# Performance work log

Measured on AMD Instinct MI355X. Metric: run time of the kernel, lower is better.

## Reference

```python
import jax, jax.numpy as jnp
import numpy as np

D_MODEL, N_HEADS, D_STATE, N_GROUPS, CHUNK = 2048, 32, 64, 1, 256
BATCH, SEQLEN = 2, 4096


def setup_inputs() -> dict:
    key = jax.random.key(0)
    ks = jax.random.split(key, 8)
    s = 0.02
    d, h, n, g = D_MODEL, N_HEADS, D_STATE, N_GROUPS
    return {
        "x": jax.random.normal(ks[0], (BATCH, SEQLEN, d), jnp.float32),
        "A_log": jnp.log(jnp.arange(1, h + 1, dtype=jnp.float32)),
        "D": jnp.ones((h,), jnp.float32),
        "B_w": jax.random.normal(ks[1], (g * n, d), jnp.float32) * s,
        "B_b": jnp.zeros((g * n,), jnp.float32),
        "C_w": jax.random.normal(ks[2], (g * n, d), jnp.float32) * s,
        "C_b": jnp.zeros((g * n,), jnp.float32),
        "dt_w": jax.random.normal(ks[3], (h, d), jnp.float32) * s,
        "dt_b": jnp.zeros((h,), jnp.float32),
        "out_w": jax.random.normal(ks[4], (d, d), jnp.float32) * s,
        "out_b": jnp.zeros((d,), jnp.float32),
    }


def segsum(v):
    # v: [..., T] -> [..., T, T]; out[i,j] = sum_{k=j+1..i} v[k] for i>=j, -inf else
    cs = jnp.cumsum(v, axis=-1)
    seg = cs[..., :, None] - cs[..., None, :]
    T = v.shape[-1]
    mask = jnp.tril(jnp.ones((T, T), bool))
    return jnp.where(mask, seg, -jnp.inf)


def _ssd(x, A_log, D, B_w, B_b, C_w, C_b, dt_w, dt_b, out_w, out_b):
    b, t, d = x.shape
    h = A_log.shape[0]
    n = B_w.shape[0] // N_GROUPS
    p = d // h
    l = CHUNK
    c = t // l

    A = -jnp.exp(A_log.astype(jnp.float32))                      # [h]
    B = (x @ B_w.T + B_b).reshape(b, t, N_GROUPS, n)             # g=1
    C = (x @ C_w.T + C_b).reshape(b, t, N_GROUPS, n)
    B = jnp.broadcast_to(B, (b, t, h, n))                        # repeat groups -> heads
    C = jnp.broadcast_to(C, (b, t, h, n))
    dt = jax.nn.softplus(x @ dt_w.T + dt_b)                      # [b,t,h]
    xh = x.reshape(b, t, h, p)

    # chunked SSD (Mamba2 mamba_chunk_scan_combined math)
    xc = xh.reshape(b, c, l, h, p)
    Bc = B.reshape(b, c, l, h, n)
    Cc = C.reshape(b, c, l, h, n)
    dtc = dt.reshape(b, c, l, h)
    dA = jnp.transpose(dtc * A, (0, 3, 1, 2))                    # [b,h,c,l]
    A_cumsum = jnp.cumsum(dA, axis=-1)                           # [b,h,c,l]

    # 1. intra-chunk (diagonal blocks)
    L = jnp.exp(segsum(dA))                                      # [b,h,c,l,l]
    xdt = xc * dtc[..., None]                                    # [b,c,l,h,p]
    Y_diag = jnp.einsum('bclhn,bcshn,bhcls,bcshp->bclhp', Cc, Bc, L, xdt)

    # 2. per-chunk final states
    decay_states = jnp.exp(A_cumsum[..., -1:] - A_cumsum)        # [b,h,c,l]
    states = jnp.einsum('bclhn,bhcl,bclhp->bchpn', Bc, decay_states, xdt)

    # 3. inter-chunk recurrence on chunk states
    states = jnp.concatenate([jnp.zeros_like(states[:, :1]), states], axis=1)  # [b,c+1,h,p,n]
    dA_last = jnp.pad(A_cumsum[..., -1], ((0, 0), (0, 0), (1, 0)))             # [b,h,c+1]
    decay_chunk = jnp.exp(segsum(dA_last))                                     # [b,h,c+1,c+1]
    new_states = jnp.einsum('bhzc,bchpn->bzhpn', decay_chunk, states)
    prev_states = new_states[:, :-1]                                           # [b,c,h,p,n]

    # 4. state -> output contribution
    state_decay_out = jnp.exp(A_cumsum)                          # [b,h,c,l]
    Y_off = jnp.einsum('bclhn,bchpn,bhcl->bclhp', Cc, prev_states, state_decay_out)

    Y = (Y_diag + Y_off).reshape(b, t, h, p) + D[None, None, :, None] * xh
    return Y.reshape(b, t, d) @ out_w.T + out_b


def reference(x, A_log, D, B_w, B_b, C_w, C_b, dt_w, dt_b, out_w, out_b):
    return _ssd(x, A_log, D, B_w, B_b, C_w, C_b, dt_w, dt_b, out_w, out_b)
```

## Files before the change

### kernel.cpp

```cpp
#include <hip/hip_runtime.h>
#include <hip/hip_bf16.h>
#include <math.h>

namespace {
constexpr int kDModel = 2048;
constexpr int kHeads  = 32;
constexpr int kState  = 64;
constexpr int kP      = 64;
constexpr int kChunk  = 256;
constexpr int kNChunk = 16;
constexpr int kBatch  = 2;
constexpr int kSeq    = 4096;
constexpr int kM      = kBatch * kSeq;
}

typedef __bf16 bf16_t;
typedef __attribute__((ext_vector_type(8))) __bf16 bf16x8;
typedef __attribute__((ext_vector_type(4))) __bf16 bf16x4;
typedef __attribute__((ext_vector_type(4))) float f32x4;

__device__ __forceinline__ void gload_lds16(const void* g, void* l) {
    __builtin_amdgcn_global_load_lds(
        (const __attribute__((address_space(1))) void*)g,
        (__attribute__((address_space(3))) void*)l,
        16, 0, 0);
}

__global__ __launch_bounds__(256)
void gemm_bcdt(const float* __restrict__ x, const bf16_t* __restrict__ W,
               const float* __restrict__ b0, const float* __restrict__ b1,
               const float* __restrict__ b2,
               bf16_t* __restrict__ o0h, bf16_t* __restrict__ o1h,
               float* __restrict__ o2f)
{
    constexpr int K = kDModel;
    __shared__ __bf16 AstS[32 * 32];
    __shared__ __bf16 WstS[160 * 32];
    const int tid  = threadIdx.x;
    const int lane = tid & 63;
    const int wave = tid >> 6;
    const int wm = (wave >> 1) * 16;
    const int wn = (wave & 1) * 80;
    const int l15 = lane & 15, quad = lane >> 4;
    const int m0 = blockIdx.x * 32;
    const int ar = tid >> 3;
    const int ac = (tid & 7) * 4;

    f32x4 acc[5];
    #pragma unroll
    for (int j = 0; j < 5; ++j) acc[j] = (f32x4){0.f, 0.f, 0.f, 0.f};

    for (int k0 = 0; k0 < K; k0 += 32) {
        const float4 av = *reinterpret_cast<const float4*>(
            x + (size_t)(m0 + ar) * K + k0 + ac);
        bf16x4 a4;
        a4[0] = (__bf16)av.x; a4[1] = (__bf16)av.y;
        a4[2] = (__bf16)av.z; a4[3] = (__bf16)av.w;
        *reinterpret_cast<bf16x4*>(&AstS[ar * 32 + ac]) = a4;
        #pragma unroll
        for (int e = 0; e < 3; ++e) {
            const int u = e * 256 + tid;
            if (u < 640)
                gload_lds16(W + (size_t)(u >> 2) * K + k0 + (u & 3) * 8, WstS + u * 8);
        }
        __syncthreads();
        bf16x8 af, bfr[5];
        af = *reinterpret_cast<const bf16x8*>(&AstS[(wm + l15) * 32 + quad * 8]);
        #pragma unroll
        for (int nf = 0; nf < 5; ++nf)
            bfr[nf] = *reinterpret_cast<const bf16x8*>(&WstS[(wn + nf * 16 + l15) * 32 + quad * 8]);
        #pragma unroll
        for (int nf = 0; nf < 5; ++nf)
            acc[nf] = __builtin_amdgcn_mfma_f32_16x16x32_bf16(af, bfr[nf], acc[nf], 0, 0, 0);
        __syncthreads();
    }

    #pragma unroll
    for (int reg = 0; reg < 4; ++reg) {
        const int r = m0 + wm + quad * 4 + reg;
        #pragma unroll
        for (int nf = 0; nf < 5; ++nf) {
            const float v = acc[nf][reg];
            const int n = wn + nf * 16 + l15;
            if (n < 64) {
                o0h[(size_t)r * 64 + n] = (bf16_t)(v + b0[n]);
            } else if (n < 128) {
                o1h[(size_t)r * 64 + (n - 64)] = (bf16_t)(v + b1[n - 64]);
            } else {
                float z = v + b2[n - 128];
                o2f[(size_t)r * 32 + (n - 128)] = (z > 20.f) ? z : log1pf(expf(z));
            }
        }
    }
}

__global__ __launch_bounds__(512, 2)
void gemm256_out(const bf16_t* __restrict__ Ap, const bf16_t* __restrict__ Bp,
                 const float* __restrict__ bias, float* __restrict__ C)
{
    constexpr int M = 8192, N = 2048, NT = 2048 / 32;
    __shared__ __bf16 Ab[3][4 * 256 * 8];
    __shared__ __bf16 Bb[3][4 * 256 * 8];
    const int tid  = threadIdx.x;
    const int lane = tid & 63;
    const int wave = tid >> 6;
    const int l15 = lane & 15, quad = lane >> 4;
    const int bid = blockIdx.x;
    const int mt = (bid & 7) * 4 + ((bid >> 3) & 3);
    const int nt = bid >> 5;
    const int m0 = mt * 256;
    const int n0 = nt * 256;
    const int wm = (wave >> 2) * 128;
    const int wn = (wave & 3) * 64;

    const int u0 = tid, u1 = tid + 512;
    auto stage = [&](int t2, int stb) {
        const int ks0 = t2 * 4;
        const bf16_t* As = Ap + ((size_t)ks0 * M + m0) * 8;
        const bf16_t* Bs = Bp + ((size_t)ks0 * N + n0) * 8;
        __bf16* Al = &Ab[stb][0];
        __bf16* Bl = &Bb[stb][0];
        gload_lds16(As + ((size_t)(u0 >> 8) * M + (u0 & 255)) * 8, Al + u0 * 8);
        gload_lds16(As + ((size_t)(u1 >> 8) * M + (u1 & 255)) * 8, Al + u1 * 8);
        gload_lds16(Bs + ((size_t)(u0 >> 8) * N + (u0 & 255)) * 8, Bl + u0 * 8);
        gload_lds16(Bs + ((size_t)(u1 >> 8) * N + (u1 & 255)) * 8, Bl + u1 * 8);
    };

    f32x4 acc[8][4];
    #pragma unroll
    for (int i = 0; i < 8; ++i)
        #pragma unroll
        for (int j = 0; j < 4; ++j)
            acc[i][j] = (f32x4){0.f, 0.f, 0.f, 0.f};

    stage(0, 0);
    stage(1, 1);
    asm volatile("s_waitcnt vmcnt(4)" ::: "memory");
    __builtin_amdgcn_s_barrier();

    int cur = 0;
    for (int t = 0; t < NT; ++t) {
        const __bf16* Ac = &Ab[cur][0];
        const __bf16* Bc = &Bb[cur][0];
        int stb = cur + 2; if (stb >= 3) stb -= 3;

        bf16x8 af[4], bfr[4];
        #pragma unroll
        for (int mi = 0; mi < 4; ++mi)
            af[mi] = *reinterpret_cast<const bf16x8*>(
                &Ac[(quad * 256 + wm + mi * 16 + l15) * 8]);
        #pragma unroll
        for (int nj = 0; nj < 4; ++nj)
            bfr[nj] = *reinterpret_cast<const bf16x8*>(
                &Bc[(quad * 256 + wn + nj * 16 + l15) * 8]);
        if (t < NT - 2) stage(t + 2, stb);
        __builtin_amdgcn_s_setprio(1);
        #pragma unroll
        for (int mi = 0; mi < 4; ++mi)
            #pragma unroll
            for (int nj = 0; nj < 4; ++nj)
                acc[mi][nj] = __builtin_amdgcn_mfma_f32_16x16x32_bf16(
                    af[mi], bfr[nj], acc[mi][nj], 0, 0, 0);
        __builtin_amdgcn_s_setprio(0);

        #pragma unroll
        for (int mi = 0; mi < 4; ++mi)
            af[mi] = *reinterpret_cast<const bf16x8*>(
                &Ac[(quad * 256 + wm + 64 + mi * 16 + l15) * 8]);
        __builtin_amdgcn_s_setprio(1);
        #pragma unroll
        for (int mi = 0; mi < 4; ++mi)
            #pragma unroll
            for (int nj = 0; nj < 4; ++nj)
                acc[4 + mi][nj] = __builtin_amdgcn_mfma_f32_16x16x32_bf16(
                    af[mi], bfr[nj], acc[4 + mi][nj], 0, 0, 0);
        __builtin_amdgcn_s_setprio(0);

        if (t < NT - 2) {
            asm volatile("s_waitcnt vmcnt(4)" ::: "memory");
        } else if (t < NT - 1) {
            asm volatile("s_waitcnt vmcnt(0)" ::: "memory");
        }
        if (t < NT - 1) __builtin_amdgcn_s_barrier();
        cur = cur + 1; if (cur == 3) cur = 0;
    }

    float bia[4];
    #pragma unroll
    for (int nj = 0; nj < 4; ++nj) bia[nj] = bias[n0 + wn + nj * 16 + l15];
    #pragma unroll
    for (int mi = 0; mi < 8; ++mi) {
        #pragma unroll
        for (int reg = 0; reg < 4; ++reg) {
            const int r = m0 + wm + mi * 16 + quad * 4 + reg;
            #pragma unroll
            for (int nj = 0; nj < 4; ++nj) {
                const int c = n0 + wn + nj * 16 + l15;
                C[(size_t)r * N + c] = acc[mi][nj][reg] + bia[nj];
            }
        }
    }
}

__global__ __launch_bounds__(256)
void prep_fused(const float* __restrict__ W, bf16_t* __restrict__ Wp,
                const float* __restrict__ B_w, const float* __restrict__ C_w,
                const float* __restrict__ dt_w, bf16_t* __restrict__ wcat)
{
    const int bid = blockIdx.x;
    if (bid < 2048) {
        const int idx = bid * 256 + threadIdx.x;
        const int n = idx >> 8, ks = idx & 255;
        const float4 v0 = *reinterpret_cast<const float4*>(W + (size_t)n * 2048 + ks * 8);
        const float4 v1 = *reinterpret_cast<const float4*>(W + (size_t)n * 2048 + ks * 8 + 4);
        bf16x8 o;
        o[0] = (__bf16)v0.x; o[1] = (__bf16)v0.y; o[2] = (__bf16)v0.z; o[3] = (__bf16)v0.w;
        o[4] = (__bf16)v1.x; o[5] = (__bf16)v1.y; o[6] = (__bf16)v1.z; o[7] = (__bf16)v1.w;
        *reinterpret_cast<bf16x8*>(Wp + ((size_t)ks * 2048 + n) * 8) = o;
    } else {
        const int idx = (bid - 2048) * 256 + threadIdx.x;
        const int r = idx >> 11, k = idx & 2047;
        float v;
        if (r < 64)       v = B_w[r * 2048 + k];
        else if (r < 128) v = C_w[(r - 64) * 2048 + k];
        else              v = dt_w[(r - 128) * 2048 + k];
        wcat[idx] = (bf16_t)v;
    }
}

__global__ __launch_bounds__(256)
void mid_fused(const float* __restrict__ dtm, const float* __restrict__ A_log,
               float* __restrict__ Acs, const bf16_t* __restrict__ Bb16,
               bf16_t* __restrict__ bTg, const float* __restrict__ x,
               bf16_t* __restrict__ xdtT)
{
    const int bid = blockIdx.x;
    const int tid = threadIdx.x;
    if (bid < 1024) {
        const int ci = bid & (kNChunk - 1);
        const int hi = (bid >> 4) & (kHeads - 1);
        const int bi = bid >> 9;
        const float Ah = -expf(A_log[hi]);
        __shared__ float s[kChunk];
        s[tid] = dtm[((size_t)bi * kSeq + ci * kChunk + tid) * kHeads + hi] * Ah;
        __syncthreads();
        for (int off = 1; off < kChunk; off <<= 1) {
            const float add = (tid >= off) ? s[tid - off] : 0.f;
            __syncthreads();
            s[tid] += add;
            __syncthreads();
        }
        Acs[((size_t)(bi * kHeads + hi) * kNChunk + ci) * kChunk + tid] = s[tid];
    } else if (bid < 1024 + 32) {
        const int blk = bid - 1024;
        const int ci = blk & (kNChunk - 1);
        const int bi = blk >> 4;
        const size_t rowbase = (size_t)bi * kSeq + ci * kChunk;
        __shared__ __bf16 T[64 * 264];
        bf16x8 v[8];
        #pragma unroll
        for (int e = 0; e < 8; ++e)
            v[e] = *reinterpret_cast<const bf16x8*>(Bb16 + (rowbase + tid) * 64 + e * 8);
        #pragma unroll
        for (int e = 0; e < 8; ++e)
            #pragma unroll
            for (int j = 0; j < 8; ++j)
                T[(e * 8 + j) * 264 + tid] = v[e][j];
        __syncthreads();
        const int n = tid >> 2, seg = (tid & 3) * 64;
        bf16_t* dst = bTg + ((size_t)(bi * kNChunk + ci)) * (64 * 256) + n * 256 + seg;
        #pragma unroll
        for (int j = 0; j < 8; ++j) {
            *reinterpret_cast<bf16x8*>(dst + j * 8) =
                *reinterpret_cast<const bf16x8*>(&T[n * 264 + seg + j * 8]);
        }
    } else {
        const int blk = bid - 1024 - 32;
        const int hi = blk & (kHeads - 1);
        const int ci = (blk >> 5) & (kNChunk - 1);
        const int bi = blk >> 9;
        const size_t rowbase = (size_t)bi * kSeq + ci * kChunk;
        __shared__ __bf16 T[64 * 264];
        const float d = dtm[(rowbase + tid) * kHeads + hi];
        const float* xs = x + (rowbase + tid) * kDModel + hi * kP;
        #pragma unroll
        for (int e = 0; e < 8; ++e) {
            const float4 a = *reinterpret_cast<const float4*>(xs + e * 8);
            const float4 b = *reinterpret_cast<const float4*>(xs + e * 8 + 4);
            T[(e * 8 + 0) * 264 + tid] = (__bf16)(a.x * d);
            T[(e * 8 + 1) * 264 + tid] = (__bf16)(a.y * d);
            T[(e * 8 + 2) * 264 + tid] = (__bf16)(a.z * d);
            T[(e * 8 + 3) * 264 + tid] = (__bf16)(a.w * d);
            T[(e * 8 + 4) * 264 + tid] = (__bf16)(b.x * d);
            T[(e * 8 + 5) * 264 + tid] = (__bf16)(b.y * d);
            T[(e * 8 + 6) * 264 + tid] = (__bf16)(b.z * d);
            T[(e * 8 + 7) * 264 + tid] = (__bf16)(b.w * d);
        }
        __syncthreads();
        const int p = tid >> 2, seg = (tid & 3) * 64;
        bf16_t* dst = xdtT + (size_t)blk * (64 * 256) + p * 256 + seg;
        #pragma unroll
        for (int j = 0; j < 8; ++j) {
            *reinterpret_cast<bf16x8*>(dst + j * 8) =
                *reinterpret_cast<const bf16x8*>(&T[p * 264 + seg + j * 8]);
        }
    }
}

__global__ __launch_bounds__(256)
void states_mfma(const bf16_t* __restrict__ xdtT, const bf16_t* __restrict__ bTg,
                 const float* __restrict__ Acs, float* __restrict__ states)
{
    const int blk = blockIdx.x;
    const int hi = blk & (kHeads - 1);
    const int ci = (blk >> 5) & (kNChunk - 1);
    const int bi = blk >> 9;
    __shared__ __bf16 Xa[64 * 264];
    __shared__ __bf16 Bt[64 * 264];
    __shared__ float dec[kChunk];
    const int tid = threadIdx.x;
    const int lane = tid & 63;
    const int wave = tid >> 6;
    const int l15 = lane & 15, quad = lane >> 4;

    const float* acs = Acs + ((size_t)(bi * kHeads + hi) * kNChunk + ci) * kChunk;
    dec[tid] = expf(acs[kChunk - 1] - acs[tid]);
    __syncthreads();

    const bf16_t* bsrc = bTg + ((size_t)(bi * kNChunk + ci)) * (64 * 256);
    const bf16_t* xsrc = xdtT + (size_t)blk * (64 * 256);
    #pragma unroll
    for (int e = 0; e < 8; ++e) {
        const int u = e * 256 + tid;
        const int r = u >> 5, seg = (u & 31) * 8;
        *reinterpret_cast<bf16x8*>(&Bt[r * 264 + seg]) =
            *reinterpret_cast<const bf16x8*>(bsrc + r * 256 + seg);
        bf16x8 xv = *reinterpret_cast<const bf16x8*>(xsrc + r * 256 + seg);
        bf16x8 xo;
        #pragma unroll
        for (int j = 0; j < 8; ++j)
            xo[j] = (__bf16)((float)xv[j] * dec[seg + j]);
        *reinterpret_cast<bf16x8*>(&Xa[r * 264 + seg]) = xo;
    }
    __syncthreads();

    f32x4 acc[4];
    #pragma unroll
    for (int ni = 0; ni < 4; ++ni) acc[ni] = (f32x4){0.f, 0.f, 0.f, 0.f};
    #pragma unroll
    for (int kk = 0; kk < 8; ++kk) {
        const bf16x8 af = *reinterpret_cast<const bf16x8*>(
            &Xa[(wave * 16 + l15) * 264 + kk * 32 + quad * 8]);
        #pragma unroll
        for (int ni = 0; ni < 4; ++ni) {
            const bf16x8 bf = *reinterpret_cast<const bf16x8*>(
                &Bt[(ni * 16 + l15) * 264 + kk * 32 + quad * 8]);
            acc[ni] = __builtin_amdgcn_mfma_f32_16x16x32_bf16(af, bf, acc[ni], 0, 0, 0);
        }
    }
    float* sp = states + (size_t)blk * (kP * kState);
    #pragma unroll
    for (int reg = 0; reg < 4; ++reg) {
        const int p = wave * 16 + quad * 4 + reg;
        #pragma unroll
        for (int ni = 0; ni < 4; ++ni)
            sp[(size_t)p * kState + ni * 16 + l15] = acc[ni][reg];
    }
}

__global__ __launch_bounds__(256)
void chunkscan_kernel(const float* __restrict__ states, const float* __restrict__ Acs,
                      bf16_t* __restrict__ prevsb)
{
    const int q  = blockIdx.x & 15;
    const int hi = (blockIdx.x >> 4) & (kHeads - 1);
    const int bi = blockIdx.x >> 9;
    const int e  = q * 256 + threadIdx.x;
    __shared__ float ea[kNChunk];
    if (threadIdx.x < kNChunk)
        ea[threadIdx.x] = expf(Acs[((size_t)(bi * kHeads + hi) * kNChunk + threadIdx.x)
                                   * kChunk + kChunk - 1]);
    __syncthreads();
    float P = 0.f;
    prevsb[((size_t)(bi * kNChunk + 0) * kHeads + hi) * (kP * kState) + e] = (bf16_t)0.f;
    for (int c = 1; c < kNChunk; ++c) {
        P = fmaf(ea[c - 1], P,
                 states[((size_t)(bi * kNChunk + (c - 1)) * kHeads + hi) * (kP * kState) + e]);
        prevsb[((size_t)(bi * kNChunk + c) * kHeads + hi) * (kP * kState) + e] = (bf16_t)P;
    }
}

__global__ __launch_bounds__(256)
void ychunk_mfma(const bf16_t* __restrict__ Bb16, const bf16_t* __restrict__ Cb16,
                 const bf16_t* __restrict__ xdtT, const float* __restrict__ Acs,
                 const bf16_t* __restrict__ prevsb, const float* __restrict__ dtm,
                 const float* __restrict__ Dvec, bf16_t* __restrict__ Yp)
{
    const int blk = blockIdx.x;
    const int lt = blk & 3;
    const int hi = (blk >> 2) & (kHeads - 1);
    const int ci = (blk >> 7) & (kNChunk - 1);
    const int bi = blk >> 11;
    __shared__ float acs_s[kChunk];
    __shared__ float dts_s[64];
    __shared__ __bf16 Cs[64 * 72];
    __shared__ __bf16 Bs[64 * 72];
    __shared__ __bf16 Xt[64 * 72];
    __shared__ __bf16 Sp[64 * 72];
    const int tid = threadIdx.x;
    const int lane = tid & 63;
    const int wave = tid >> 6;
    const int l15 = lane & 15, quad = lane >> 4;
    const int mrow = wave * 16 + quad * 4;
    const size_t rowbase = (size_t)bi * kSeq + ci * kChunk;
    const bf16_t* xdsrc = xdtT + ((size_t)((bi * kNChunk + ci) * kHeads + hi)) * (64 * 256);

    acs_s[tid] = Acs[((size_t)(bi * kHeads + hi) * kNChunk + ci) * kChunk + tid];
    if (tid < 64) dts_s[tid] = dtm[(rowbase + lt * 64 + tid) * kHeads + hi];
    const bf16_t* pp = prevsb + ((size_t)(bi * kNChunk + ci) * kHeads + hi) * (kP * kState);
    #pragma unroll
    for (int e = 0; e < 2; ++e) {
        const int u = e * 256 + tid;
        const int r = u >> 3, seg = (u & 7) * 8;
        *reinterpret_cast<bf16x8*>(&Cs[r * 72 + seg]) =
            *reinterpret_cast<const bf16x8*>(Cb16 + (rowbase + lt * 64 + r) * 64 + seg);
        *reinterpret_cast<bf16x8*>(&Bs[r * 72 + seg]) =
            *reinterpret_cast<const bf16x8*>(pp + r * 64 + seg);
    }
    __syncthreads();

    bf16x8 af[2];
    af[0] = *reinterpret_cast<const bf16x8*>(&Cs[(wave * 16 + l15) * 72 + quad * 8]);
    af[1] = *reinterpret_cast<const bf16x8*>(&Cs[(wave * 16 + l15) * 72 + 32 + quad * 8]);

    f32x4 yacc[4];
    #pragma unroll
    for (int ni = 0; ni < 4; ++ni) yacc[ni] = (f32x4){0.f, 0.f, 0.f, 0.f};
    #pragma unroll
    for (int ni = 0; ni < 4; ++ni) {
        const bf16x8 b0 = *reinterpret_cast<const bf16x8*>(&Bs[(ni * 16 + l15) * 72 + quad * 8]);
        const bf16x8 b1 = *reinterpret_cast<const bf16x8*>(&Bs[(ni * 16 + l15) * 72 + 32 + quad * 8]);
        yacc[ni] = __builtin_amdgcn_mfma_f32_16x16x32_bf16(af[0], b0, yacc[ni], 0, 0, 0);
        yacc[ni] = __builtin_amdgcn_mfma_f32_16x16x32_bf16(af[1], b1, yacc[ni], 0, 0, 0);
    }
    {
        float es[4];
        #pragma unroll
        for (int reg = 0; reg < 4; ++reg) es[reg] = expf(acs_s[lt * 64 + mrow + reg]);
        #pragma unroll
        for (int ni = 0; ni < 4; ++ni)
            #pragma unroll
            for (int reg = 0; reg < 4; ++reg) yacc[ni][reg] *= es[reg];
    }

    for (int st = 0; st <= lt; ++st) {
        __syncthreads();
        #pragma unroll
        for (int e = 0; e < 2; ++e) {
            const int u = e * 256 + tid;
            const int r = u >> 3, seg = (u & 7) * 8;
            *reinterpret_cast<bf16x8*>(&Bs[r * 72 + seg]) =
                *reinterpret_cast<const bf16x8*>(Bb16 + (rowbase + st * 64 + r) * 64 + seg);
            *reinterpret_cast<bf16x8*>(&Xt[r * 72 + seg]) =
                *reinterpret_cast<const bf16x8*>(xdsrc + r * 256 + st * 64 + seg);
        }
        __syncthreads();
        f32x4 sacc[4];
        #pragma unroll
        for (int ni = 0; ni < 4; ++ni) sacc[ni] = (f32x4){0.f, 0.f, 0.f, 0.f};
        #pragma unroll
        for (int ni = 0; ni < 4; ++ni) {
            const bf16x8 b0 = *reinterpret_cast<const bf16x8*>(&Bs[(ni * 16 + l15) * 72 + quad * 8]);
            const bf16x8 b1 = *reinterpret_cast<const bf16x8*>(&Bs[(ni * 16 + l15) * 72 + 32 + quad * 8]);
            sacc[ni] = __builtin_amdgcn_mfma_f32_16x16x32_bf16(af[0], b0, sacc[ni], 0, 0, 0);
            sacc[ni] = __builtin_amdgcn_mfma_f32_16x16x32_bf16(af[1], b1, sacc[ni], 0, 0, 0);
        }
        #pragma unroll
        for (int reg = 0; reg < 4; ++reg) {
            const int l = lt * 64 + mrow + reg;
            const float al = acs_s[l];
            #pragma unroll
            for (int ni = 0; ni < 4; ++ni) {
                const int scol = ni * 16 + l15;
                const int sg = st * 64 + scol;
                float v = sacc[ni][reg] * expf(al - acs_s[sg]);
                if (st == lt && sg > l) v = 0.f;
                Sp[(mrow + reg) * 72 + scol] = (__bf16)v;
            }
        }
        asm volatile("s_waitcnt lgkmcnt(0)" ::: "memory");
        __builtin_amdgcn_sched_barrier(0);
        const bf16x8 as0 = *reinterpret_cast<const bf16x8*>(&Sp[(wave * 16 + l15) * 72 + quad * 8]);
        const bf16x8 as1 = *reinterpret_cast<const bf16x8*>(&Sp[(wave * 16 + l15) * 72 + 32 + quad * 8]);
        #pragma unroll
        for (int ni = 0; ni < 4; ++ni) {
            const bf16x8 x0 = *reinterpret_cast<const bf16x8*>(&Xt[(ni * 16 + l15) * 72 + quad * 8]);
            const bf16x8 x1 = *reinterpret_cast<const bf16x8*>(&Xt[(ni * 16 + l15) * 72 + 32 + quad * 8]);
            yacc[ni] = __builtin_amdgcn_mfma_f32_16x16x32_bf16(as0, x0, yacc[ni], 0, 0, 0);
            yacc[ni] = __builtin_amdgcn_mfma_f32_16x16x32_bf16(as1, x1, yacc[ni], 0, 0, 0);
        }
    }

    const float Dh = Dvec[hi];
    #pragma unroll
    for (int reg = 0; reg < 4; ++reg) {
        const int lrow = mrow + reg;
        const size_t tg = rowbase + lt * 64 + lrow;
        const float dinv = 1.f / dts_s[lrow];
        #pragma unroll
        for (int ni = 0; ni < 4; ++ni) {
            const int p = ni * 16 + l15;
            const float xv = (float)Xt[p * 72 + lrow] * dinv;
            const float v = yacc[ni][reg] + Dh * xv;
            Yp[((size_t)(hi * 8 + (p >> 3)) * (size_t)kM + tg) * 8 + (p & 7)] = (bf16_t)v;
        }
    }
}

extern "C" void kernel_launch(void* const* d_in, const int* in_sizes, int n_in,
                              void* d_out, int out_size, void* d_ws, size_t ws_size,
                              hipStream_t stream)
{
    (void)in_sizes; (void)n_in; (void)out_size; (void)ws_size;
    const float* x     = (const float*)d_in[0];
    const float* A_log = (const float*)d_in[1];
    const float* Dvec  = (const float*)d_in[2];
    const float* B_w   = (const float*)d_in[3];
    const float* B_b   = (const float*)d_in[4];
    const float* C_w   = (const float*)d_in[5];
    const float* C_b   = (const float*)d_in[6];
    const float* dt_w  = (const float*)d_in[7];
    const float* dt_b  = (const float*)d_in[8];
    const float* out_w = (const float*)d_in[9];
    const float* out_b = (const float*)d_in[10];
    float* out = (float*)d_out;

    float* ws = (float*)d_ws;
    float* dtm    = ws;
    float* Acs    = dtm + (size_t)kM * kHeads;
    float* states = Acs + (size_t)kBatch * kHeads * kNChunk * kChunk;
    bf16_t* prevsb = (bf16_t*)(states + (size_t)kBatch * kNChunk * kHeads * kP * kState);
    bf16_t* Y     = prevsb + (size_t)kBatch * kNChunk * kHeads * kP * kState;
    bf16_t* Bb16  = Y + (size_t)kM * kDModel;
    bf16_t* Cb16  = Bb16 + (size_t)kM * kState;
    bf16_t* xdtT  = Cb16 + (size_t)kM * kState;
    bf16_t* bTg   = xdtT + (size_t)kM * kDModel;
    bf16_t* wcat  = bTg + (size_t)kBatch * kNChunk * kState * kChunk;
    bf16_t* wob   = wcat + (size_t)160 * kDModel;

    const dim3 blk(256);
    prep_fused<<<dim3(2048 + 1280), blk, 0, stream>>>(out_w, wob, B_w, C_w, dt_w, wcat);
    gemm_bcdt<<<dim3(kM / 32), blk, 0, stream>>>(x, wcat, B_b, C_b, dt_b,
                                                 Bb16, Cb16, dtm);
    mid_fused<<<dim3(1024 + 32 + 1024), blk, 0, stream>>>(
        dtm, A_log, Acs, Bb16, bTg, x, xdtT);
    states_mfma<<<dim3(kBatch * kNChunk * kHeads), blk, 0, stream>>>(xdtT, bTg, Acs, states);
    chunkscan_kernel<<<dim3(kBatch * kHeads * 16), blk, 0, stream>>>(states, Acs, prevsb);
    ychunk_mfma<<<dim3(kBatch * kNChunk * kHeads * 4), blk, 0, stream>>>(
        Bb16, Cb16, xdtT, Acs, prevsb, dtm, Dvec, Y);
    gemm256_out<<<dim3(256), dim3(512), 0, stream>>>(Y, wob, out_b, out);
}
```

Before: 356.3 us.

## Triple-buffer BCdt GEMM via direct LDS loads and register-prefetch ychunk tiles

```diff
diff --git a/kernel.cpp b/kernel.cpp
--- a/kernel.cpp
+++ b/kernel.cpp
@@ -34,8 +34,9 @@
                float* __restrict__ o2f)
 {
     constexpr int K = kDModel;
-    __shared__ __bf16 AstS[32 * 32];
-    __shared__ __bf16 WstS[160 * 32];
+    constexpr int NT = K / 32;
+    __shared__ float  Ast[3][256 * 4];
+    __shared__ __bf16 Wst[3][768 * 8];
     const int tid  = threadIdx.x;
     const int lane = tid & 63;
     const int wave = tid >> 6;
@@ -43,36 +44,63 @@
     const int wn = (wave & 1) * 80;
     const int l15 = lane & 15, quad = lane >> 4;
     const int m0 = blockIdx.x * 32;
-    const int ar = tid >> 3;
-    const int ac = (tid & 7) * 4;
-
-    f32x4 acc[5];
-    #pragma unroll
-    for (int j = 0; j < 5; ++j) acc[j] = (f32x4){0.f, 0.f, 0.f, 0.f};
-
-    for (int k0 = 0; k0 < K; k0 += 32) {
-        const float4 av = *reinterpret_cast<const float4*>(
-            x + (size_t)(m0 + ar) * K + k0 + ac);
-        bf16x4 a4;
-        a4[0] = (__bf16)av.x; a4[1] = (__bf16)av.y;
-        a4[2] = (__bf16)av.z; a4[3] = (__bf16)av.w;
-        *reinterpret_cast<bf16x4*>(&AstS[ar * 32 + ac]) = a4;
+    const int aks = tid >> 5, arow = tid & 31;
+
+    auto stage = [&](int t2, int sb) {
+        const int k0 = t2 * 32;
+        gload_lds16(x + (size_t)(m0 + arow) * K + k0 + aks * 4, &Ast[sb][tid * 4]);
         #pragma unroll
         for (int e = 0; e < 3; ++e) {
             const int u = e * 256 + tid;
-            if (u < 640)
-                gload_lds16(W + (size_t)(u >> 2) * K + k0 + (u & 3) * 8, WstS + u * 8);
-        }
-        __syncthreads();
-        bf16x8 af, bfr[5];
-        af = *reinterpret_cast<const bf16x8*>(&AstS[(wm + l15) * 32 + quad * 8]);
+            const int ks = u / 192;
+            const int n  = u - ks * 192;
+            gload_lds16(W + (size_t)n * K + k0 + ks * 8, &Wst[sb][u * 8]);
+        }
+    };
+
+    f32x4 acc[5];
+    #pragma unroll
+    for (int j = 0; j < 5; ++j) acc[j] = (f32x4){0.f, 0.f, 0.f, 0.f};
+
+    stage(0, 0);
+    stage(1, 1);
+    asm volatile("s_waitcnt vmcnt(4)" ::: "memory");
+    __builtin_amdgcn_s_barrier();
+
+    int cur = 0;
+    for (int t = 0; t < NT; ++t) {
+        const float*  Ac = &Ast[cur][0];
+        const __bf16* Wc = &Wst[cur][0];
+        int stb = cur + 2; if (stb >= 3) stb -= 3;
+
+        const float4 a0 = *reinterpret_cast<const float4*>(
+            &Ac[((quad * 2 + 0) * 32 + wm + l15) * 4]);
+        const float4 a1 = *reinterpret_cast<const float4*>(
+            &Ac[((quad * 2 + 1) * 32 + wm + l15) * 4]);
+        bf16x8 af;
+        af[0] = (__bf16)a0.x; af[1] = (__bf16)a0.y;
+        af[2] = (__bf16)a0.z; af[3] = (__bf16)a0.w;
+        af[4] = (__bf16)a1.x; af[5] = (__bf16)a1.y;
+        af[6] = (__bf16)a1.z; af[7] = (__bf16)a1.w;
+        bf16x8 bfr[5];
         #pragma unroll
         for (int nf = 0; nf < 5; ++nf)
-            bfr[nf] = *reinterpret_cast<const bf16x8*>(&WstS[(wn + nf * 16 + l15) * 32 + quad * 8]);
+            bfr[nf] = *reinterpret_cast<const bf16x8*>(
+                &Wc[(quad * 192 + wn + nf * 16 + l15) * 8]);
+        if (t < NT - 2) stage(t + 2, stb);
+        __builtin_amdgcn_s_setprio(1);
         #pragma unroll
         for (int nf = 0; nf < 5; ++nf)
             acc[nf] = __builtin_amdgcn_mfma_f32_16x16x32_bf16(af, bfr[nf], acc[nf], 0, 0, 0);
-        __syncthreads();
+        __builtin_amdgcn_s_setprio(0);
+
+        if (t < NT - 2) {
+            asm volatile("s_waitcnt vmcnt(4)" ::: "memory");
+        } else if (t < NT - 1) {
+            asm volatile("s_waitcnt vmcnt(0)" ::: "memory");
+        }
+        if (t < NT - 1) __builtin_amdgcn_s_barrier();
+        cur = cur + 1; if (cur == 3) cur = 0;
     }
 
     #pragma unroll
@@ -220,10 +248,10 @@
     } else {
         const int idx = (bid - 2048) * 256 + threadIdx.x;
         const int r = idx >> 11, k = idx & 2047;
-        float v;
+        float v = 0.f;
         if (r < 64)       v = B_w[r * 2048 + k];
         else if (r < 128) v = C_w[(r - 64) * 2048 + k];
-        else              v = dt_w[(r - 128) * 2048 + k];
+        else if (r < 160) v = dt_w[(r - 128) * 2048 + k];
         wcat[idx] = (bf16_t)v;
     }
 }
@@ -414,19 +442,25 @@
     const int mrow = wave * 16 + quad * 4;
     const size_t rowbase = (size_t)bi * kSeq + ci * kChunk;
     const bf16_t* xdsrc = xdtT + ((size_t)((bi * kNChunk + ci) * kHeads + hi)) * (64 * 256);
+    const int ur0 = tid >> 3,          useg0 = (tid & 7) * 8;
+    const int ur1 = (256 + tid) >> 3,  useg1 = (tid & 7) * 8;
 
     acs_s[tid] = Acs[((size_t)(bi * kHeads + hi) * kNChunk + ci) * kChunk + tid];
     if (tid < 64) dts_s[tid] = dtm[(rowbase + lt * 64 + tid) * kHeads + hi];
     const bf16_t* pp = prevsb + ((size_t)(bi * kNChunk + ci) * kHeads + hi) * (kP * kState);
     #pragma unroll
     for (int e = 0; e < 2; ++e) {
-        const int u = e * 256 + tid;
-        const int r = u >> 3, seg = (u & 7) * 8;
+        const int r = e ? ur1 : ur0, seg = e ? useg1 : useg0;
         *reinterpret_cast<bf16x8*>(&Cs[r * 72 + seg]) =
             *reinterpret_cast<const bf16x8*>(Cb16 + (rowbase + lt * 64 + r) * 64 + seg);
         *reinterpret_cast<bf16x8*>(&Bs[r * 72 + seg]) =
             *reinterpret_cast<const bf16x8*>(pp + r * 64 + seg);
     }
+    bf16x8 rB0, rB1, rX0, rX1;
+    rB0 = *reinterpret_cast<const bf16x8*>(Bb16 + (rowbase + ur0) * 64 + useg0);
+    rB1 = *reinterpret_cast<const bf16x8*>(Bb16 + (rowbase + ur1) * 64 + useg1);
+    rX0 = *reinterpret_cast<const bf16x8*>(xdsrc + ur0 * 256 + useg0);
+    rX1 = *reinterpret_cast<const bf16x8*>(xdsrc + ur1 * 256 + useg1);
     __syncthreads();
 
     bf16x8 af[2];
@@ -455,14 +489,15 @@
 
     for (int st = 0; st <= lt; ++st) {
         __syncthreads();
-        #pragma unroll
-        for (int e = 0; e < 2; ++e) {
-            const int u = e * 256 + tid;
-            const int r = u >> 3, seg = (u & 7) * 8;
-            *reinterpret_cast<bf16x8*>(&Bs[r * 72 + seg]) =
-                *reinterpret_cast<const bf16x8*>(Bb16 + (rowbase + st * 64 + r) * 64 + seg);
-            *reinterpret_cast<bf16x8*>(&Xt[r * 72 + seg]) =
-                *reinterpret_cast<const bf16x8*>(xdsrc + r * 256 + st * 64 + seg);
+        *reinterpret_cast<bf16x8*>(&Bs[ur0 * 72 + useg0]) = rB0;
+        *reinterpret_cast<bf16x8*>(&Bs[ur1 * 72 + useg1]) = rB1;
+        *reinterpret_cast<bf16x8*>(&Xt[ur0 * 72 + useg0]) = rX0;
+        *reinterpret_cast<bf16x8*>(&Xt[ur1 * 72 + useg1]) = rX1;
+        if (st < lt) {
+            rB0 = *reinterpret_cast<const bf16x8*>(Bb16 + (rowbase + (st + 1) * 64 + ur0) * 64 + useg0);
+            rB1 = *reinterpret_cast<const bf16x8*>(Bb16 + (rowbase + (st + 1) * 64 + ur1) * 64 + useg1);
+            rX0 = *reinterpret_cast<const bf16x8*>(xdsrc + ur0 * 256 + (st + 1) * 64 + useg0);
+            rX1 = *reinterpret_cast<const bf16x8*>(xdsrc + ur1 * 256 + (st + 1) * 64 + useg1);
         }
         __syncthreads();
         f32x4 sacc[4];
@@ -546,10 +581,10 @@
     bf16_t* xdtT  = Cb16 + (size_t)kM * kState;
     bf16_t* bTg   = xdtT + (size_t)kM * kDModel;
     bf16_t* wcat  = bTg + (size_t)kBatch * kNChunk * kState * kChunk;
-    bf16_t* wob   = wcat + (size_t)160 * kDModel;
+    bf16_t* wob   = wcat + (size_t)192 * kDModel;
 
     const dim3 blk(256);
-    prep_fused<<<dim3(2048 + 1280), blk, 0, stream>>>(out_w, wob, B_w, C_w, dt_w, wcat);
+    prep_fused<<<dim3(2048 + 1536), blk, 0, stream>>>(out_w, wob, B_w, C_w, dt_w, wcat);
     gemm_bcdt<<<dim3(kM / 32), blk, 0, stream>>>(x, wcat, B_b, C_b, dt_b,
                                                  Bb16, Cb16, dtm);
     mid_fused<<<dim3(1024 + 32 + 1024), blk, 0, stream>>>(
```

Result: no change. 350.6 us (-1.6%).
